# Performance work log

Hardware: AMD Instinct MI355X
Metric: run time of the kernel (lower is better)

Reference implementation:

```python
import jax, jax.numpy as jnp
import numpy as np

N = 4096
INPUT_DIM = 512
KEY_DIM = 64
OUT_DIM = 512
N_HEADS = 8


def _xavier_normal(key, shape, gain):
    # torch xavier_normal_ on [heads, fan_in, fan_out]: fan over last two dims
    fan_in, fan_out = shape[-2], shape[-1]
    std = gain * (2.0 / (fan_in + fan_out)) ** 0.5
    return jax.random.normal(key, shape, dtype=jnp.float32) * std


def setup_inputs() -> dict:
    key = jax.random.key(0)
    kx, ka, kk, kq, kv, ko = jax.random.split(key, 6)
    gain = 2.0 ** 0.5
    node_matrix = jax.random.normal(kx, (N, INPUT_DIM), dtype=jnp.float32)
    adjacency_matrix = jax.random.randint(ka, (N, N), 0, 2).astype(jnp.float32)
    Wks = _xavier_normal(kk, (N_HEADS, INPUT_DIM, KEY_DIM), gain)
    Wqs = _xavier_normal(kq, (N_HEADS, INPUT_DIM, KEY_DIM), gain)
    Wvs = _xavier_normal(kv, (N_HEADS, INPUT_DIM, KEY_DIM), gain)
    Wo = _xavier_normal(ko, (N_HEADS, KEY_DIM, OUT_DIM), gain)
    return {"node_matrix": node_matrix, "adjacency_matrix": adjacency_matrix,
            "Wks": Wks, "Wqs": Wqs, "Wvs": Wvs, "Wo": Wo}


def reference(node_matrix, adjacency_matrix, Wks, Wqs, Wvs, Wo):
    n = adjacency_matrix.shape[0]
    # force self-loops
    adj = jnp.maximum(adjacency_matrix, jnp.eye(n, dtype=adjacency_matrix.dtype))
    # per-head projections: [heads, N, key_dim]
    keys = jnp.einsum('nj,hjk->hnk', node_matrix, Wks)
    queries = jnp.einsum('nj,hjk->hnk', node_matrix, Wqs)
    values = jnp.einsum('nj,hjk->hnk', node_matrix, Wvs)
    key_dim = Wks.shape[-1]
    # [heads, N(query), N(key)] scores, scaled and adjacency-masked
    atts = jnp.einsum('hqk,hmk->hqm', queries, keys) / (key_dim ** 0.5)
    atts = atts - 1e16 * (1.0 - adj)[None, :, :]
    atts = jax.nn.softmax(atts, axis=-1)
    # weighted values, then output projection, summed over heads -> [N, out_dim]
    return jnp.einsum('hqm,hmk,hko->qo', atts, values, Wo)
```

## Files before the change

### kernel.cpp

```cpp
#include <hip/hip_runtime.h>
#include <stdint.h>

typedef unsigned short u16;
typedef __attribute__((ext_vector_type(8))) __bf16 bf16x8;
typedef __attribute__((ext_vector_type(8))) short short8;
typedef __attribute__((ext_vector_type(4))) float f32x4;

#define N_NODES 4096
#define DMODEL  512
#define QKVLD   1536
#define KD      64
#define NH      8
#define LOG2E   1.4426950408889634f

static __device__ __forceinline__ u16 f2bf(float f) {
  unsigned u = __builtin_bit_cast(unsigned, f);
  u += 0x7fffu + ((u >> 16) & 1u);
  return (u16)(u >> 16);
}

static __device__ __forceinline__ f32x4 mfma16(short8 a, short8 b, f32x4 c) {
  return __builtin_amdgcn_mfma_f32_16x16x32_bf16(
      __builtin_bit_cast(bf16x8, a), __builtin_bit_cast(bf16x8, b), c, 0, 0, 0);
}

static __device__ __forceinline__ void gload16(const u16* g, u16* l) {
  __builtin_amdgcn_global_load_lds((const __attribute__((address_space(1))) void*)g,
                                   (__attribute__((address_space(3))) void*)l, 16, 0, 0);
}


__global__ void conv_bf16(const float* __restrict__ in, u16* __restrict__ out, int n4) {
  int i = blockIdx.x * blockDim.x + threadIdx.x;
  if (i < n4) {
    float4 v = ((const float4*)in)[i];
    ushort4 o; o.x = f2bf(v.x); o.y = f2bf(v.y); o.z = f2bf(v.z); o.w = f2bf(v.w);
    ((ushort4*)out)[i] = o;
  }
}

__global__ void pack_qkv(const float* __restrict__ Wq, const float* __restrict__ Wk,
                         const float* __restrict__ Wv, u16* __restrict__ Wt) {
  __shared__ float t[64][65];
  int z = blockIdx.z;
  int mat = z >> 3, h = z & 7;
  const float* src = (mat == 0) ? Wq : ((mat == 1) ? Wk : Wv);
  float scale = (mat == 0) ? 0.125f * LOG2E : 1.0f;
  src += (size_t)h * DMODEL * KD;
  u16* dst = Wt + ((size_t)mat * DMODEL + (size_t)h * KD) * DMODEL;
  int r0 = blockIdx.x * 64;
  int tid = threadIdx.x, lc = tid & 63;
#pragma unroll
  for (int i = 0; i < 16; ++i) {
    int row = i * 4 + (tid >> 6);
    t[row][lc] = src[(size_t)(r0 + row) * KD + lc];
  }
  __syncthreads();
#pragma unroll
  for (int i = 0; i < 16; ++i) {
    int row = i * 4 + (tid >> 6);
    dst[(size_t)row * DMODEL + r0 + lc] = f2bf(t[lc][row] * scale);
  }
}

__global__ void pack_wo(const float* __restrict__ Wo, u16* __restrict__ Wot) {
  __shared__ float t[64][65];
  int r0 = blockIdx.x * 64, c0 = blockIdx.y * 64;
  int tid = threadIdx.x, lc = tid & 63;
#pragma unroll
  for (int i = 0; i < 16; ++i) {
    int row = i * 4 + (tid >> 6);
    t[row][lc] = Wo[(size_t)(r0 + row) * 512 + c0 + lc];
  }
  __syncthreads();
#pragma unroll
  for (int i = 0; i < 16; ++i) {
    int row = i * 4 + (tid >> 6);
    Wot[(size_t)(c0 + row) * 512 + r0 + lc] = f2bf(t[lc][row]);
  }
}

__global__ void build_bits(const float* __restrict__ adj, unsigned long long* __restrict__ bits) {
  int gw = (blockIdx.x * blockDim.x + threadIdx.x) >> 6;
  int lane = threadIdx.x & 63;
  int nw = (gridDim.x * blockDim.x) >> 6;
  for (int word = gw; word < N_NODES * 64; word += nw) {
    int q = word >> 6, wc = word & 63;
    int k = wc * 64 + lane;
    float v = adj[(size_t)q * N_NODES + k];
    unsigned long long m = __ballot((v != 0.0f) || (q == k));
    if (lane == 0) bits[word] = m;
  }
}

__global__ void vtrans(const u16* __restrict__ QKV, u16* __restrict__ Vt) {
  __shared__ u16 t[64][65];
  int n0 = blockIdx.x * 64, h = blockIdx.y;
  int tid = threadIdx.x, lc = tid & 63;
#pragma unroll
  for (int i = 0; i < 16; ++i) {
    int row = i * 4 + (tid >> 6);
    t[row][lc] = QKV[(size_t)(n0 + row) * QKVLD + 1024 + h * 64 + lc];
  }
  __syncthreads();
#pragma unroll
  for (int i = 0; i < 16; ++i) {
    int d = i * 4 + (tid >> 6);
    Vt[((size_t)h * 64 + d) * N_NODES + n0 + lc] = t[lc][d];
  }
}

template <bool OUT_BF16>
__global__ __launch_bounds__(256) void gemm_nt(const u16* __restrict__ A,
                                               const u16* __restrict__ Bt,
                                               void* __restrict__ C, int K,
                                               int lda, int ldb, int ldc) {
  __shared__ __align__(16) u16 lA[64 * 64];
  __shared__ __align__(16) u16 lB[64 * 64];
  const int m0 = blockIdx.x * 64, n0 = blockIdx.y * 64;
  const int tid = threadIdx.x;
  const int w = tid >> 6, lane = tid & 63, lm = lane & 15, lg = lane >> 4;
  const int srow = tid >> 2, sc0 = tid & 3;
  f32x4 acc[4] = {};
  for (int k0 = 0; k0 < K; k0 += 64) {
    __syncthreads();
    {
      const short8* ga = (const short8*)(A + (size_t)(m0 + srow) * lda + k0);
      short8* la = (short8*)(lA + srow * 64);
      la[sc0 ^ (srow & 7)] = ga[sc0];
      la[(sc0 + 4) ^ (srow & 7)] = ga[sc0 + 4];
      const short8* gb = (const short8*)(Bt + (size_t)(n0 + srow) * ldb + k0);
      short8* lb = (short8*)(lB + srow * 64);
      lb[sc0 ^ (srow & 7)] = gb[sc0];
      lb[(sc0 + 4) ^ (srow & 7)] = gb[sc0 + 4];
    }
    __syncthreads();
    short8 af0, af1;
    {
      int row = w * 16 + lm;
      af0 = ((short8*)(lA + row * 64))[lg ^ (row & 7)];
      af1 = ((short8*)(lA + row * 64))[(4 + lg) ^ (row & 7)];
    }
#pragma unroll
    for (int nt = 0; nt < 4; ++nt) {
      int row = nt * 16 + lm;
      short8 b0 = ((short8*)(lB + row * 64))[lg ^ (row & 7)];
      short8 b1 = ((short8*)(lB + row * 64))[(4 + lg) ^ (row & 7)];
      acc[nt] = mfma16(af0, b0, acc[nt]);
      acc[nt] = mfma16(af1, b1, acc[nt]);
    }
  }
#pragma unroll
  for (int nt = 0; nt < 4; ++nt) {
#pragma unroll
    for (int r = 0; r < 4; ++r) {
      int m = m0 + w * 16 + lg * 4 + r;
      int n = n0 + nt * 16 + lm;
      if (OUT_BF16)
        ((u16*)C)[(size_t)m * ldc + n] = f2bf(acc[nt][r]);
      else
        ((float*)C)[(size_t)m * ldc + n] = acc[nt][r];
    }
  }
}

__global__ __launch_bounds__(256, 2) void attn_kernel(const u16* __restrict__ QKV,
                                                      const u16* __restrict__ Vt,
                                                      const unsigned long long* __restrict__ bits,
                                                      float* __restrict__ Op,
                                                      float* __restrict__ lp) {
  __shared__ __align__(16) u16 lK[2][64 * 64];
  __shared__ __align__(16) u16 lV[2][64 * 64];
  __shared__ __align__(16) u16 lP[4][2][16 * 64];
  const int bid = blockIdx.x;
  const int h = bid & 7, sp = (bid >> 3) & 1, qb = bid >> 4;
  const int tid = threadIdx.x;
  const int w = tid >> 6, lane = tid & 63, lm = lane & 15, lg = lane >> 4;
  const int lg4 = lg * 4;
  const int kb0 = sp * 32;

  const int q0 = qb * 128 + w * 32 + lm;
  const int q1 = q0 + 16;

  const short8 qf00 = *(const short8*)(QKV + (size_t)q0 * QKVLD + h * 64 + lg * 8);
  const short8 qf01 = *(const short8*)(QKV + (size_t)q0 * QKVLD + h * 64 + 32 + lg * 8);
  const short8 qf10 = *(const short8*)(QKV + (size_t)q1 * QKVLD + h * 64 + lg * 8);
  const short8 qf11 = *(const short8*)(QKV + (size_t)q1 * QKVLD + h * 64 + 32 + lg * 8);

  short8 ones;
#pragma unroll
  for (int j = 0; j < 8; ++j) ones[j] = (short)0x3F80;

  const int srow = lane >> 3, sc = lane & 7;
  const u16* kP[2]; const u16* vP[2];
#pragma unroll
  for (int i = 0; i < 2; ++i) {
    int row = w * 16 + i * 8 + srow;
    kP[i] = QKV + (size_t)(kb0 * 64 + row) * QKVLD + 512 + h * 64 + (sc ^ (row & 7)) * 8;
    vP[i] = Vt + ((size_t)h * 64 + row) * N_NODES + kb0 * 64 + (sc ^ (row & 7)) * 8;
  }

#define STAGE(buf) do {                                   \
    gload16(kP[0], &lK[buf][(w * 2 + 0) * 512]);          \
    gload16(kP[1], &lK[buf][(w * 2 + 1) * 512]);          \
    gload16(vP[0], &lV[buf][(w * 2 + 0) * 512]);          \
    gload16(vP[1], &lV[buf][(w * 2 + 1) * 512]);          \
  } while (0)
#define ADV() do { kP[0] += 64 * QKVLD; kP[1] += 64 * QKVLD; vP[0] += 64; vP[1] += 64; } while (0)

  f32x4 of0[4] = {}, of1[4] = {};
  f32x4 la0 = {}, la1 = {};
  const unsigned long long* bp0 = bits + (size_t)q0 * 64 + kb0;
  const unsigned long long* bp1 = bits + (size_t)q1 * 64 + kb0;

  STAGE(0);
  unsigned long long wb0 = bp0[0], wb1 = bp1[0];

  char* Pw0 = (char*)lP[w][0];
  char* Pw1 = (char*)lP[w][1];
  const int pswz = (lm & 7) << 4;

#define SMPACK(sv, wbv, Pw, la)                                                \
  do {                                                                         \
    unsigned wlo = (unsigned)((wbv) >> lg4);                                   \
    unsigned whi = (unsigned)((wbv) >> (lg4 + 32));                            \
    _Pragma("unroll")                                                          \
    for (int kt = 0; kt < 4; ++kt) {                                           \
      float pv[4];                                                             \
      unsigned word = (kt < 2) ? wlo : whi;                                    \
      _Pragma("unroll")                                                        \
      for (int r = 0; r < 4; ++r) {                                            \
        float e = __builtin_exp2f(sv[kt][r]);                                  \
        int pos = (kt & 1) * 16 + r;                                           \
        unsigned mb = (unsigned)((int)(word << (31 - pos)) >> 31);             \
        pv[r] = __builtin_bit_cast(float, __builtin_bit_cast(unsigned, e) & mb); \
      }                                                                        \
      unsigned pk0, pk1;                                                       \
      asm("v_cvt_pk_bf16_f32 %0, %1, %2" : "=v"(pk0) : "v"(pv[0]), "v"(pv[1]));\
      asm("v_cvt_pk_bf16_f32 %0, %1, %2" : "=v"(pk1) : "v"(pv[2]), "v"(pv[3]));\
      uint2 pr; pr.x = pk0; pr.y = pk1;                                        \
      *(uint2*)(Pw + lm * 128 + ((kt * 32 + lg * 8) ^ pswz)) = pr;             \
    }                                                                          \
    short8 pa0 = *(const short8*)(Pw + lm * 128 + ((lg * 16) ^ pswz));         \
    short8 pa1 = *(const short8*)(Pw + lm * 128 + ((64 + lg * 16) ^ pswz));    \
    la = mfma16(ones, pa0, la);                                                \
    la = mfma16(ones, pa1, la);                                                \
    _Pragma("unroll")                                                          \
    for (int dt = 0; dt < 4; ++dt) {                                           \
      int row = dt * 16 + lm;                                                  \
      short8 v0 = ((const short8*)(lVc + row * 64))[lg ^ (row & 7)];           \
      short8 v1 = ((const short8*)(lVc + row * 64))[(4 + lg) ^ (row & 7)];     \
      OFA[dt] = mfma16(v0, pa0, OFA[dt]);                                      \
      OFA[dt] = mfma16(v1, pa1, OFA[dt]);                                      \
    }                                                                          \
  } while (0)

#define BODY(cur, i)                                                           \
  do {                                                                         \
    asm volatile("s_waitcnt vmcnt(0)" ::: "memory");                           \
    __builtin_amdgcn_s_barrier();                                              \
    if ((i) + 1 < 32) { ADV(); STAGE(cur ^ 1); }                               \
    unsigned long long nb0 = ((i) + 1 < 32) ? bp0[(i) + 1] : 0ull;             \
    unsigned long long nb1 = ((i) + 1 < 32) ? bp1[(i) + 1] : 0ull;             \
    const u16* lKc = lK[cur];                                                  \
    const u16* lVc = lV[cur];                                                  \
    f32x4 s0[4], s1[4];                                                        \
    _Pragma("unroll")                                                          \
    for (int kt = 0; kt < 4; ++kt) {                                           \
      int row = kt * 16 + lm;                                                  \
      short8 k0 = ((const short8*)(lKc + row * 64))[lg ^ (row & 7)];           \
      short8 k1 = ((const short8*)(lKc + row * 64))[(4 + lg) ^ (row & 7)];     \
      f32x4 z0 = {0.f, 0.f, 0.f, 0.f}, z1 = {0.f, 0.f, 0.f, 0.f};              \
      z0 = mfma16(k0, qf00, z0); s0[kt] = mfma16(k1, qf01, z0);                \
      z1 = mfma16(k0, qf10, z1); s1[kt] = mfma16(k1, qf11, z1);                \
    }                                                                          \
    { f32x4* OFA = of0; SMPACK(s0, wb0, Pw0, la0); }                           \
    { f32x4* OFA = of1; SMPACK(s1, wb1, Pw1, la1); }                           \
    wb0 = nb0; wb1 = nb1;                                                      \
  } while (0)

#pragma unroll 1
  for (int it = 0; it < 16; ++it) {
    BODY(0, it * 2);
    BODY(1, it * 2 + 1);
  }
#undef BODY
#undef SMPACK
#undef STAGE
#undef ADV

  float* Ob = Op + (size_t)sp * N_NODES * DMODEL;
#pragma unroll
  for (int dt = 0; dt < 4; ++dt) {
    *(f32x4*)(Ob + (size_t)q0 * DMODEL + h * 64 + dt * 16 + lg4) = of0[dt];
    *(f32x4*)(Ob + (size_t)q1 * DMODEL + h * 64 + dt * 16 + lg4) = of1[dt];
  }
  if (lg == 0) {
    lp[((size_t)sp * NH + h) * N_NODES + q0] = la0[0];
    lp[((size_t)sp * NH + h) * N_NODES + q1] = la1[0];
  }
}

__global__ __launch_bounds__(256) void combine_kernel(const float* __restrict__ Op,
                                                      const float* __restrict__ lp,
                                                      u16* __restrict__ Oc) {
  int i = blockIdx.x * 256 + threadIdx.x;
  int col = (i * 4) & (DMODEL - 1);
  int q = (i * 4) >> 9;
  int h = col >> 6;
  float4 a = ((const float4*)Op)[i];
  float4 b = ((const float4*)(Op + (size_t)N_NODES * DMODEL))[i];
  float l = lp[(size_t)h * N_NODES + q] + lp[((size_t)NH + h) * N_NODES + q];
  float inv = 1.0f / l;
  ushort4 o;
  o.x = f2bf((a.x + b.x) * inv);
  o.y = f2bf((a.y + b.y) * inv);
  o.z = f2bf((a.z + b.z) * inv);
  o.w = f2bf((a.w + b.w) * inv);
  ((ushort4*)Oc)[i] = o;
}


extern "C" void kernel_launch(void* const* d_in, const int* in_sizes, int n_in,
                              void* d_out, int out_size, void* d_ws, size_t ws_size,
                              hipStream_t stream) {
  const float* X   = (const float*)d_in[0];
  const float* Adj = (const float*)d_in[1];
  const float* Wks = (const float*)d_in[2];
  const float* Wqs = (const float*)d_in[3];
  const float* Wvs = (const float*)d_in[4];
  const float* Wo  = (const float*)d_in[5];

  char* p = (char*)d_ws;
  u16* Xb  = (u16*)p; p += (size_t)N_NODES * DMODEL * 2;
  u16* Wt  = (u16*)p; p += (size_t)3 * DMODEL * DMODEL * 2;
  u16* Wot = (u16*)p; p += (size_t)DMODEL * DMODEL * 2;
  u16* QKV = (u16*)p; p += (size_t)N_NODES * QKVLD * 2;
  u16* Vt  = (u16*)p; p += (size_t)N_NODES * DMODEL * 2;
  u16* Oc  = (u16*)p; p += (size_t)N_NODES * DMODEL * 2;
  unsigned long long* bits = (unsigned long long*)p; p += (size_t)N_NODES * 64 * 8;
  float* Op = (float*)p; p += (size_t)2 * N_NODES * DMODEL * 4;
  float* lp = (float*)p; p += (size_t)2 * NH * N_NODES * 4;

  conv_bf16<<<dim3(2048), dim3(256), 0, stream>>>(X, Xb, N_NODES * DMODEL / 4);
  pack_qkv<<<dim3(8, 1, 24), dim3(256), 0, stream>>>(Wqs, Wks, Wvs, Wt);
  pack_wo<<<dim3(8, 8), dim3(256), 0, stream>>>(Wo, Wot);
  build_bits<<<dim3(2048), dim3(256), 0, stream>>>(Adj, bits);

  gemm_nt<true><<<dim3(64, 24), dim3(256), 0, stream>>>(Xb, Wt, QKV, 512, 512, 512, QKVLD);
  vtrans<<<dim3(64, 8), dim3(256), 0, stream>>>(QKV, Vt);

  attn_kernel<<<dim3(512), dim3(256), 0, stream>>>(QKV, Vt, bits, Op, lp);
  combine_kernel<<<dim3(N_NODES * DMODEL / 4 / 256), dim3(256), 0, stream>>>(Op, lp, Oc);

  gemm_nt<false><<<dim3(64, 8), dim3(256), 0, stream>>>(Oc, Wot, d_out, 512, 512, 512, 512);
}
```

Measured before the change: 132.8 us.

## Raise attention query tile to 64 rows per wave, split keys 4 ways, fuse V transpose

Each wave in the attention kernel now handles 64 query rows instead of 32, so every K/V tile loaded into LDS is reused across four query sub-tiles. The key dimension is split four ways instead of two, which keeps the grid at 512 blocks, and the combine kernel sums four partials. The separate V-transpose kernel is removed: the QKV GEMM epilogue now writes transposed V directly. The costs are higher register pressure (16 output accumulators per lane), double the partial-output traffic, and scattered transposed stores from the GEMM epilogue.

```diff
diff --git a/kernel.cpp b/kernel.cpp
--- a/kernel.cpp
+++ b/kernel.cpp
@@ -11,6 +11,7 @@
 #define QKVLD   1536
 #define KD      64
 #define NH      8
+#define NSPLIT  4
 #define LOG2E   1.4426950408889634f
 
 static __device__ __forceinline__ u16 f2bf(float f) {
@@ -93,28 +94,12 @@
   }
 }
 
-__global__ void vtrans(const u16* __restrict__ QKV, u16* __restrict__ Vt) {
-  __shared__ u16 t[64][65];
-  int n0 = blockIdx.x * 64, h = blockIdx.y;
-  int tid = threadIdx.x, lc = tid & 63;
-#pragma unroll
-  for (int i = 0; i < 16; ++i) {
-    int row = i * 4 + (tid >> 6);
-    t[row][lc] = QKV[(size_t)(n0 + row) * QKVLD + 1024 + h * 64 + lc];
-  }
-  __syncthreads();
-#pragma unroll
-  for (int i = 0; i < 16; ++i) {
-    int d = i * 4 + (tid >> 6);
-    Vt[((size_t)h * 64 + d) * N_NODES + n0 + lc] = t[lc][d];
-  }
-}
-
 template <bool OUT_BF16>
 __global__ __launch_bounds__(256) void gemm_nt(const u16* __restrict__ A,
                                                const u16* __restrict__ Bt,
                                                void* __restrict__ C, int K,
-                                               int lda, int ldb, int ldc) {
+                                               int lda, int ldb, int ldc,
+                                               u16* __restrict__ Vt) {
   __shared__ __align__(16) u16 lA[64 * 64];
   __shared__ __align__(16) u16 lB[64 * 64];
   const int m0 = blockIdx.x * 64, n0 = blockIdx.y * 64;
@@ -152,14 +137,20 @@
   }
 #pragma unroll
   for (int nt = 0; nt < 4; ++nt) {
-#pragma unroll
-    for (int r = 0; r < 4; ++r) {
-      int m = m0 + w * 16 + lg * 4 + r;
-      int n = n0 + nt * 16 + lm;
-      if (OUT_BF16)
-        ((u16*)C)[(size_t)m * ldc + n] = f2bf(acc[nt][r]);
-      else
-        ((float*)C)[(size_t)m * ldc + n] = acc[nt][r];
+    int n = n0 + nt * 16 + lm;
+    int mb = m0 + w * 16 + lg * 4;
+    if (OUT_BF16) {
+      ushort4 o4;
+#pragma unroll
+      for (int r = 0; r < 4; ++r) ((u16*)&o4)[r] = f2bf(acc[nt][r]);
+#pragma unroll
+      for (int r = 0; r < 4; ++r) ((u16*)C)[(size_t)(mb + r) * ldc + n] = ((u16*)&o4)[r];
+      if (Vt != nullptr && n >= 1024)
+        *(ushort4*)(Vt + (size_t)(n - 1024) * N_NODES + mb) = o4;
+    } else {
+#pragma unroll
+      for (int r = 0; r < 4; ++r)
+        ((float*)C)[(size_t)(mb + r) * ldc + n] = acc[nt][r];
     }
   }
 }
@@ -173,19 +164,20 @@
   __shared__ __align__(16) u16 lV[2][64 * 64];
   __shared__ __align__(16) u16 lP[4][2][16 * 64];
   const int bid = blockIdx.x;
-  const int h = bid & 7, sp = (bid >> 3) & 1, qb = bid >> 4;
+  const int h = bid & 7, sp = (bid >> 3) & 3, qb = bid >> 5;
   const int tid = threadIdx.x;
   const int w = tid >> 6, lane = tid & 63, lm = lane & 15, lg = lane >> 4;
   const int lg4 = lg * 4;
-  const int kb0 = sp * 32;
-
-  const int q0 = qb * 128 + w * 32 + lm;
-  const int q1 = q0 + 16;
-
-  const short8 qf00 = *(const short8*)(QKV + (size_t)q0 * QKVLD + h * 64 + lg * 8);
-  const short8 qf01 = *(const short8*)(QKV + (size_t)q0 * QKVLD + h * 64 + 32 + lg * 8);
-  const short8 qf10 = *(const short8*)(QKV + (size_t)q1 * QKVLD + h * 64 + lg * 8);
-  const short8 qf11 = *(const short8*)(QKV + (size_t)q1 * QKVLD + h * 64 + 32 + lg * 8);
+  const int kb0 = sp * 16;
+  const int q0 = qb * 256 + w * 64 + lm;
+
+  short8 qf[4][2];
+#pragma unroll
+  for (int s = 0; s < 4; ++s) {
+    const u16* qp = QKV + (size_t)(q0 + 16 * s) * QKVLD + h * 64;
+    qf[s][0] = *(const short8*)(qp + lg * 8);
+    qf[s][1] = *(const short8*)(qp + 32 + lg * 8);
+  }
 
   short8 ones;
 #pragma unroll
@@ -208,96 +200,99 @@
   } while (0)
 #define ADV() do { kP[0] += 64 * QKVLD; kP[1] += 64 * QKVLD; vP[0] += 64; vP[1] += 64; } while (0)
 
-  f32x4 of0[4] = {}, of1[4] = {};
-  f32x4 la0 = {}, la1 = {};
-  const unsigned long long* bp0 = bits + (size_t)q0 * 64 + kb0;
-  const unsigned long long* bp1 = bits + (size_t)q1 * 64 + kb0;
+  f32x4 of[4][4] = {};
+  f32x4 la[4] = {};
+  const unsigned long long* bp[4];
+#pragma unroll
+  for (int s = 0; s < 4; ++s) bp[s] = bits + (size_t)(q0 + 16 * s) * 64 + kb0;
 
   STAGE(0);
-  unsigned long long wb0 = bp0[0], wb1 = bp1[0];
-
-  char* Pw0 = (char*)lP[w][0];
-  char* Pw1 = (char*)lP[w][1];
+  unsigned long long wb[4];
+#pragma unroll
+  for (int s = 0; s < 4; ++s) wb[s] = bp[s][0];
+
   const int pswz = (lm & 7) << 4;
 
-#define SMPACK(sv, wbv, Pw, la)                                                \
-  do {                                                                         \
-    unsigned wlo = (unsigned)((wbv) >> lg4);                                   \
-    unsigned whi = (unsigned)((wbv) >> (lg4 + 32));                            \
-    _Pragma("unroll")                                                          \
-    for (int kt = 0; kt < 4; ++kt) {                                           \
-      float pv[4];                                                             \
-      unsigned word = (kt < 2) ? wlo : whi;                                    \
-      _Pragma("unroll")                                                        \
-      for (int r = 0; r < 4; ++r) {                                            \
-        float e = __builtin_exp2f(sv[kt][r]);                                  \
-        int pos = (kt & 1) * 16 + r;                                           \
-        unsigned mb = (unsigned)((int)(word << (31 - pos)) >> 31);             \
-        pv[r] = __builtin_bit_cast(float, __builtin_bit_cast(unsigned, e) & mb); \
-      }                                                                        \
-      unsigned pk0, pk1;                                                       \
-      asm("v_cvt_pk_bf16_f32 %0, %1, %2" : "=v"(pk0) : "v"(pv[0]), "v"(pv[1]));\
-      asm("v_cvt_pk_bf16_f32 %0, %1, %2" : "=v"(pk1) : "v"(pv[2]), "v"(pv[3]));\
-      uint2 pr; pr.x = pk0; pr.y = pk1;                                        \
-      *(uint2*)(Pw + lm * 128 + ((kt * 32 + lg * 8) ^ pswz)) = pr;             \
-    }                                                                          \
-    short8 pa0 = *(const short8*)(Pw + lm * 128 + ((lg * 16) ^ pswz));         \
-    short8 pa1 = *(const short8*)(Pw + lm * 128 + ((64 + lg * 16) ^ pswz));    \
-    la = mfma16(ones, pa0, la);                                                \
-    la = mfma16(ones, pa1, la);                                                \
-    _Pragma("unroll")                                                          \
-    for (int dt = 0; dt < 4; ++dt) {                                           \
-      int row = dt * 16 + lm;                                                  \
-      short8 v0 = ((const short8*)(lVc + row * 64))[lg ^ (row & 7)];           \
-      short8 v1 = ((const short8*)(lVc + row * 64))[(4 + lg) ^ (row & 7)];     \
-      OFA[dt] = mfma16(v0, pa0, OFA[dt]);                                      \
-      OFA[dt] = mfma16(v1, pa1, OFA[dt]);                                      \
-    }                                                                          \
-  } while (0)
-
-#define BODY(cur, i)                                                           \
-  do {                                                                         \
-    asm volatile("s_waitcnt vmcnt(0)" ::: "memory");                           \
-    __builtin_amdgcn_s_barrier();                                              \
-    if ((i) + 1 < 32) { ADV(); STAGE(cur ^ 1); }                               \
-    unsigned long long nb0 = ((i) + 1 < 32) ? bp0[(i) + 1] : 0ull;             \
-    unsigned long long nb1 = ((i) + 1 < 32) ? bp1[(i) + 1] : 0ull;             \
-    const u16* lKc = lK[cur];                                                  \
-    const u16* lVc = lV[cur];                                                  \
-    f32x4 s0[4], s1[4];                                                        \
-    _Pragma("unroll")                                                          \
-    for (int kt = 0; kt < 4; ++kt) {                                           \
-      int row = kt * 16 + lm;                                                  \
-      short8 k0 = ((const short8*)(lKc + row * 64))[lg ^ (row & 7)];           \
-      short8 k1 = ((const short8*)(lKc + row * 64))[(4 + lg) ^ (row & 7)];     \
-      f32x4 z0 = {0.f, 0.f, 0.f, 0.f}, z1 = {0.f, 0.f, 0.f, 0.f};              \
-      z0 = mfma16(k0, qf00, z0); s0[kt] = mfma16(k1, qf01, z0);                \
-      z1 = mfma16(k0, qf10, z1); s1[kt] = mfma16(k1, qf11, z1);                \
-    }                                                                          \
-    { f32x4* OFA = of0; SMPACK(s0, wb0, Pw0, la0); }                           \
-    { f32x4* OFA = of1; SMPACK(s1, wb1, Pw1, la1); }                           \
-    wb0 = nb0; wb1 = nb1;                                                      \
-  } while (0)
-
-#pragma unroll 1
+#pragma unroll 2
   for (int it = 0; it < 16; ++it) {
-    BODY(0, it * 2);
-    BODY(1, it * 2 + 1);
-  }
-#undef BODY
-#undef SMPACK
+    asm volatile("s_waitcnt vmcnt(0)" ::: "memory");
+    __builtin_amdgcn_s_barrier();
+    const int cur = it & 1;
+    if (it + 1 < 16) { ADV(); STAGE(cur ^ 1); }
+    unsigned long long nb[4];
+#pragma unroll
+    for (int s = 0; s < 4; ++s) nb[s] = (it + 1 < 16) ? bp[s][it + 1] : 0ull;
+
+    const u16* lKc = lK[cur];
+    const u16* lVc = lV[cur];
+
+    short8 kf[4][2];
+#pragma unroll
+    for (int kt = 0; kt < 4; ++kt) {
+      int row = kt * 16 + lm;
+      kf[kt][0] = ((const short8*)(lKc + row * 64))[lg ^ (row & 7)];
+      kf[kt][1] = ((const short8*)(lKc + row * 64))[(4 + lg) ^ (row & 7)];
+    }
+
+    short8 pa[4][2];
+#pragma unroll
+    for (int s = 0; s < 4; ++s) {
+      f32x4 ss[4];
+#pragma unroll
+      for (int kt = 0; kt < 4; ++kt) {
+        f32x4 z = {};
+        z = mfma16(kf[kt][0], qf[s][0], z);
+        ss[kt] = mfma16(kf[kt][1], qf[s][1], z);
+      }
+      unsigned wlo = (unsigned)(wb[s] >> lg4);
+      unsigned whi = (unsigned)(wb[s] >> (lg4 + 32));
+      char* Pw = (char*)lP[w][s & 1];
+#pragma unroll
+      for (int kt = 0; kt < 4; ++kt) {
+        float pv[4];
+        unsigned word = (kt < 2) ? wlo : whi;
+#pragma unroll
+        for (int r = 0; r < 4; ++r) {
+          float e = __builtin_exp2f(ss[kt][r]);
+          int pos = (kt & 1) * 16 + r;
+          unsigned mb = (unsigned)((int)(word << (31 - pos)) >> 31);
+          pv[r] = __builtin_bit_cast(float, __builtin_bit_cast(unsigned, e) & mb);
+        }
+        unsigned pk0, pk1;
+        asm("v_cvt_pk_bf16_f32 %0, %1, %2" : "=v"(pk0) : "v"(pv[0]), "v"(pv[1]));
+        asm("v_cvt_pk_bf16_f32 %0, %1, %2" : "=v"(pk1) : "v"(pv[2]), "v"(pv[3]));
+        uint2 pr; pr.x = pk0; pr.y = pk1;
+        *(uint2*)(Pw + lm * 128 + ((kt * 32 + lg * 8) ^ pswz)) = pr;
+      }
+      pa[s][0] = *(const short8*)(Pw + lm * 128 + ((lg * 16) ^ pswz));
+      pa[s][1] = *(const short8*)(Pw + lm * 128 + ((64 + lg * 16) ^ pswz));
+      la[s] = mfma16(ones, pa[s][0], la[s]);
+      la[s] = mfma16(ones, pa[s][1], la[s]);
+      wb[s] = nb[s];
+    }
+
+#pragma unroll
+    for (int dt = 0; dt < 4; ++dt) {
+      int row = dt * 16 + lm;
+      short8 v0 = ((const short8*)(lVc + row * 64))[lg ^ (row & 7)];
+      short8 v1 = ((const short8*)(lVc + row * 64))[(4 + lg) ^ (row & 7)];
+#pragma unroll
+      for (int s = 0; s < 4; ++s) {
+        of[s][dt] = mfma16(v0, pa[s][0], of[s][dt]);
+        of[s][dt] = mfma16(v1, pa[s][1], of[s][dt]);
+      }
+    }
+  }
 #undef STAGE
 #undef ADV
 
   float* Ob = Op + (size_t)sp * N_NODES * DMODEL;
 #pragma unroll
-  for (int dt = 0; dt < 4; ++dt) {
-    *(f32x4*)(Ob + (size_t)q0 * DMODEL + h * 64 + dt * 16 + lg4) = of0[dt];
-    *(f32x4*)(Ob + (size_t)q1 * DMODEL + h * 64 + dt * 16 + lg4) = of1[dt];
-  }
-  if (lg == 0) {
-    lp[((size_t)sp * NH + h) * N_NODES + q0] = la0[0];
-    lp[((size_t)sp * NH + h) * N_NODES + q1] = la1[0];
+  for (int s = 0; s < 4; ++s) {
+#pragma unroll
+    for (int dt = 0; dt < 4; ++dt)
+      *(f32x4*)(Ob + (size_t)(q0 + 16 * s) * DMODEL + h * 64 + dt * 16 + lg4) = of[s][dt];
+    if (lg == 0) lp[((size_t)sp * NH + h) * N_NODES + q0 + 16 * s] = la[s][0];
   }
 }
 
@@ -308,15 +303,20 @@
   int col = (i * 4) & (DMODEL - 1);
   int q = (i * 4) >> 9;
   int h = col >> 6;
-  float4 a = ((const float4*)Op)[i];
-  float4 b = ((const float4*)(Op + (size_t)N_NODES * DMODEL))[i];
-  float l = lp[(size_t)h * N_NODES + q] + lp[((size_t)NH + h) * N_NODES + q];
+  float4 acc = {0.f, 0.f, 0.f, 0.f};
+  float l = 0.f;
+#pragma unroll
+  for (int sp = 0; sp < NSPLIT; ++sp) {
+    float4 a = ((const float4*)(Op + (size_t)sp * N_NODES * DMODEL))[i];
+    acc.x += a.x; acc.y += a.y; acc.z += a.z; acc.w += a.w;
+    l += lp[((size_t)sp * NH + h) * N_NODES + q];
+  }
   float inv = 1.0f / l;
   ushort4 o;
-  o.x = f2bf((a.x + b.x) * inv);
-  o.y = f2bf((a.y + b.y) * inv);
-  o.z = f2bf((a.z + b.z) * inv);
-  o.w = f2bf((a.w + b.w) * inv);
+  o.x = f2bf(acc.x * inv);
+  o.y = f2bf(acc.y * inv);
+  o.z = f2bf(acc.z * inv);
+  o.w = f2bf(acc.w * inv);
   ((ushort4*)Oc)[i] = o;
 }
 
@@ -339,19 +339,18 @@
   u16* Vt  = (u16*)p; p += (size_t)N_NODES * DMODEL * 2;
   u16* Oc  = (u16*)p; p += (size_t)N_NODES * DMODEL * 2;
   unsigned long long* bits = (unsigned long long*)p; p += (size_t)N_NODES * 64 * 8;
-  float* Op = (float*)p; p += (size_t)2 * N_NODES * DMODEL * 4;
-  float* lp = (float*)p; p += (size_t)2 * NH * N_NODES * 4;
+  float* Op = (float*)p; p += (size_t)NSPLIT * N_NODES * DMODEL * 4;
+  float* lp = (float*)p; p += (size_t)NSPLIT * NH * N_NODES * 4;
 
   conv_bf16<<<dim3(2048), dim3(256), 0, stream>>>(X, Xb, N_NODES * DMODEL / 4);
   pack_qkv<<<dim3(8, 1, 24), dim3(256), 0, stream>>>(Wqs, Wks, Wvs, Wt);
   pack_wo<<<dim3(8, 8), dim3(256), 0, stream>>>(Wo, Wot);
   build_bits<<<dim3(2048), dim3(256), 0, stream>>>(Adj, bits);
 
-  gemm_nt<true><<<dim3(64, 24), dim3(256), 0, stream>>>(Xb, Wt, QKV, 512, 512, 512, QKVLD);
-  vtrans<<<dim3(64, 8), dim3(256), 0, stream>>>(QKV, Vt);
+  gemm_nt<true><<<dim3(64, 24), dim3(256), 0, stream>>>(Xb, Wt, QKV, 512, 512, 512, QKVLD, Vt);
 
   attn_kernel<<<dim3(512), dim3(256), 0, stream>>>(QKV, Vt, bits, Op, lp);
   combine_kernel<<<dim3(N_NODES * DMODEL / 4 / 256), dim3(256), 0, stream>>>(Op, lp, Oc);
 
-  gemm_nt<false><<<dim3(64, 8), dim3(256), 0, stream>>>(Oc, Wot, d_out, 512, 512, 512, 512);
-}
+  gemm_nt<false><<<dim3(64, 8), dim3(256), 0, stream>>>(Oc, Wot, d_out, 512, 512, 512, 512, nullptr);
+}
```

After: 137.2 us. 3.3% more time.

## Split attention keys four ways and fuse V transpose into QKV GEMM epilogue

Applied to the files above, without the earlier changes.

Raises the key-dimension split of the attention kernel from two to four, doubling the grid to 1024 blocks and targeting four blocks per CU by shrinking the per-wave P scratch buffer. The V transpose kernel is removed; the QKV GEMM epilogue now also writes the transposed V directly. The combine kernel sums four partial outputs, which adds more fp32 partial-result traffic and memory in exchange for better occupancy and one fewer launch.

```diff
diff --git a/kernel.cpp b/kernel.cpp
--- a/kernel.cpp
+++ b/kernel.cpp
@@ -11,6 +11,7 @@
 #define QKVLD   1536
 #define KD      64
 #define NH      8
+#define NSPLIT  4
 #define LOG2E   1.4426950408889634f
 
 static __device__ __forceinline__ u16 f2bf(float f) {
@@ -93,28 +94,12 @@
   }
 }
 
-__global__ void vtrans(const u16* __restrict__ QKV, u16* __restrict__ Vt) {
-  __shared__ u16 t[64][65];
-  int n0 = blockIdx.x * 64, h = blockIdx.y;
-  int tid = threadIdx.x, lc = tid & 63;
-#pragma unroll
-  for (int i = 0; i < 16; ++i) {
-    int row = i * 4 + (tid >> 6);
-    t[row][lc] = QKV[(size_t)(n0 + row) * QKVLD + 1024 + h * 64 + lc];
-  }
-  __syncthreads();
-#pragma unroll
-  for (int i = 0; i < 16; ++i) {
-    int d = i * 4 + (tid >> 6);
-    Vt[((size_t)h * 64 + d) * N_NODES + n0 + lc] = t[lc][d];
-  }
-}
-
 template <bool OUT_BF16>
 __global__ __launch_bounds__(256) void gemm_nt(const u16* __restrict__ A,
                                                const u16* __restrict__ Bt,
                                                void* __restrict__ C, int K,
-                                               int lda, int ldb, int ldc) {
+                                               int lda, int ldb, int ldc,
+                                               u16* __restrict__ Vt) {
   __shared__ __align__(16) u16 lA[64 * 64];
   __shared__ __align__(16) u16 lB[64 * 64];
   const int m0 = blockIdx.x * 64, n0 = blockIdx.y * 64;
@@ -152,32 +137,38 @@
   }
 #pragma unroll
   for (int nt = 0; nt < 4; ++nt) {
-#pragma unroll
-    for (int r = 0; r < 4; ++r) {
-      int m = m0 + w * 16 + lg * 4 + r;
-      int n = n0 + nt * 16 + lm;
-      if (OUT_BF16)
-        ((u16*)C)[(size_t)m * ldc + n] = f2bf(acc[nt][r]);
-      else
-        ((float*)C)[(size_t)m * ldc + n] = acc[nt][r];
+    int n = n0 + nt * 16 + lm;
+    int mb = m0 + w * 16 + lg * 4;
+    if (OUT_BF16) {
+      ushort4 o4;
+#pragma unroll
+      for (int r = 0; r < 4; ++r) ((u16*)&o4)[r] = f2bf(acc[nt][r]);
+#pragma unroll
+      for (int r = 0; r < 4; ++r) ((u16*)C)[(size_t)(mb + r) * ldc + n] = ((u16*)&o4)[r];
+      if (Vt != nullptr && n >= 1024)
+        *(ushort4*)(Vt + (size_t)(n - 1024) * N_NODES + mb) = o4;
+    } else {
+#pragma unroll
+      for (int r = 0; r < 4; ++r)
+        ((float*)C)[(size_t)(mb + r) * ldc + n] = acc[nt][r];
     }
   }
 }
 
-__global__ __launch_bounds__(256, 2) void attn_kernel(const u16* __restrict__ QKV,
+__global__ __launch_bounds__(256, 4) void attn_kernel(const u16* __restrict__ QKV,
                                                       const u16* __restrict__ Vt,
                                                       const unsigned long long* __restrict__ bits,
                                                       float* __restrict__ Op,
                                                       float* __restrict__ lp) {
   __shared__ __align__(16) u16 lK[2][64 * 64];
   __shared__ __align__(16) u16 lV[2][64 * 64];
-  __shared__ __align__(16) u16 lP[4][2][16 * 64];
+  __shared__ __align__(16) u16 lP[4][16 * 64];
   const int bid = blockIdx.x;
-  const int h = bid & 7, sp = (bid >> 3) & 1, qb = bid >> 4;
+  const int h = bid & 7, sp = (bid >> 3) & 3, qb = bid >> 5;
   const int tid = threadIdx.x;
   const int w = tid >> 6, lane = tid & 63, lm = lane & 15, lg = lane >> 4;
   const int lg4 = lg * 4;
-  const int kb0 = sp * 32;
+  const int kb0 = sp * 16;
 
   const int q0 = qb * 128 + w * 32 + lm;
   const int q1 = q0 + 16;
@@ -216,11 +207,10 @@
   STAGE(0);
   unsigned long long wb0 = bp0[0], wb1 = bp1[0];
 
-  char* Pw0 = (char*)lP[w][0];
-  char* Pw1 = (char*)lP[w][1];
+  char* Pw = (char*)lP[w];
   const int pswz = (lm & 7) << 4;
 
-#define SMPACK(sv, wbv, Pw, la)                                                \
+#define SMPACK(sv, wbv, la, OFA)                                               \
   do {                                                                         \
     unsigned wlo = (unsigned)((wbv) >> lg4);                                   \
     unsigned whi = (unsigned)((wbv) >> (lg4 + 32));                            \
@@ -259,9 +249,9 @@
   do {                                                                         \
     asm volatile("s_waitcnt vmcnt(0)" ::: "memory");                           \
     __builtin_amdgcn_s_barrier();                                              \
-    if ((i) + 1 < 32) { ADV(); STAGE(cur ^ 1); }                               \
-    unsigned long long nb0 = ((i) + 1 < 32) ? bp0[(i) + 1] : 0ull;             \
-    unsigned long long nb1 = ((i) + 1 < 32) ? bp1[(i) + 1] : 0ull;             \
+    if ((i) + 1 < 16) { ADV(); STAGE(cur ^ 1); }                               \
+    unsigned long long nb0 = ((i) + 1 < 16) ? bp0[(i) + 1] : 0ull;             \
+    unsigned long long nb1 = ((i) + 1 < 16) ? bp1[(i) + 1] : 0ull;             \
     const u16* lKc = lK[cur];                                                  \
     const u16* lVc = lV[cur];                                                  \
     f32x4 s0[4], s1[4];                                                        \
@@ -274,13 +264,13 @@
       z0 = mfma16(k0, qf00, z0); s0[kt] = mfma16(k1, qf01, z0);                \
       z1 = mfma16(k0, qf10, z1); s1[kt] = mfma16(k1, qf11, z1);                \
     }                                                                          \
-    { f32x4* OFA = of0; SMPACK(s0, wb0, Pw0, la0); }                           \
-    { f32x4* OFA = of1; SMPACK(s1, wb1, Pw1, la1); }                           \
+    SMPACK(s0, wb0, la0, of0);                                                 \
+    SMPACK(s1, wb1, la1, of1);                                                 \
     wb0 = nb0; wb1 = nb1;                                                      \
   } while (0)
 
 #pragma unroll 1
-  for (int it = 0; it < 16; ++it) {
+  for (int it = 0; it < 8; ++it) {
     BODY(0, it * 2);
     BODY(1, it * 2 + 1);
   }
@@ -308,15 +298,20 @@
   int col = (i * 4) & (DMODEL - 1);
   int q = (i * 4) >> 9;
   int h = col >> 6;
-  float4 a = ((const float4*)Op)[i];
-  float4 b = ((const float4*)(Op + (size_t)N_NODES * DMODEL))[i];
-  float l = lp[(size_t)h * N_NODES + q] + lp[((size_t)NH + h) * N_NODES + q];
+  float4 acc = {0.f, 0.f, 0.f, 0.f};
+  float l = 0.f;
+#pragma unroll
+  for (int sp = 0; sp < NSPLIT; ++sp) {
+    float4 a = ((const float4*)(Op + (size_t)sp * N_NODES * DMODEL))[i];
+    acc.x += a.x; acc.y += a.y; acc.z += a.z; acc.w += a.w;
+    l += lp[((size_t)sp * NH + h) * N_NODES + q];
+  }
   float inv = 1.0f / l;
   ushort4 o;
-  o.x = f2bf((a.x + b.x) * inv);
-  o.y = f2bf((a.y + b.y) * inv);
-  o.z = f2bf((a.z + b.z) * inv);
-  o.w = f2bf((a.w + b.w) * inv);
+  o.x = f2bf(acc.x * inv);
+  o.y = f2bf(acc.y * inv);
+  o.z = f2bf(acc.z * inv);
+  o.w = f2bf(acc.w * inv);
   ((ushort4*)Oc)[i] = o;
 }
 
@@ -339,19 +334,18 @@
   u16* Vt  = (u16*)p; p += (size_t)N_NODES * DMODEL * 2;
   u16* Oc  = (u16*)p; p += (size_t)N_NODES * DMODEL * 2;
   unsigned long long* bits = (unsigned long long*)p; p += (size_t)N_NODES * 64 * 8;
-  float* Op = (float*)p; p += (size_t)2 * N_NODES * DMODEL * 4;
-  float* lp = (float*)p; p += (size_t)2 * NH * N_NODES * 4;
+  float* Op = (float*)p; p += (size_t)NSPLIT * N_NODES * DMODEL * 4;
+  float* lp = (float*)p; p += (size_t)NSPLIT * NH * N_NODES * 4;
 
   conv_bf16<<<dim3(2048), dim3(256), 0, stream>>>(X, Xb, N_NODES * DMODEL / 4);
   pack_qkv<<<dim3(8, 1, 24), dim3(256), 0, stream>>>(Wqs, Wks, Wvs, Wt);
   pack_wo<<<dim3(8, 8), dim3(256), 0, stream>>>(Wo, Wot);
   build_bits<<<dim3(2048), dim3(256), 0, stream>>>(Adj, bits);
 
-  gemm_nt<true><<<dim3(64, 24), dim3(256), 0, stream>>>(Xb, Wt, QKV, 512, 512, 512, QKVLD);
-  vtrans<<<dim3(64, 8), dim3(256), 0, stream>>>(QKV, Vt);
-
-  attn_kernel<<<dim3(512), dim3(256), 0, stream>>>(QKV, Vt, bits, Op, lp);
+  gemm_nt<true><<<dim3(64, 24), dim3(256), 0, stream>>>(Xb, Wt, QKV, 512, 512, 512, QKVLD, Vt);
+
+  attn_kernel<<<dim3(1024), dim3(256), 0, stream>>>(QKV, Vt, bits, Op, lp);
   combine_kernel<<<dim3(N_NODES * DMODEL / 4 / 256), dim3(256), 0, stream>>>(Op, lp, Oc);
 
-  gemm_nt<false><<<dim3(64, 8), dim3(256), 0, stream>>>(Oc, Wot, d_out, 512, 512, 512, 512);
-}
+  gemm_nt<false><<<dim3(64, 8), dim3(256), 0, stream>>>(Oc, Wot, d_out, 512, 512, 512, 512, nullptr);
+}
```

Result: slower. 139.5 us (+5.0%).
